# Performance work log

Measured on AMD Instinct MI355X. Metric: run time of the kernel, lower is better.

## Reference

```python
import jax, jax.numpy as jnp
import numpy as np

TEMPERATURE = 8.0  # sqrt(d_k=64)
NEG_INF = -1000000000.0

B, H, S, D = 2, 16, 2048, 64


def setup_inputs() -> dict:
    key = jax.random.key(0)
    kq, kk, kv, knm, km = jax.random.split(key, 5)
    q = jax.random.normal(kq, (B, H, S, D), dtype=jnp.float32)
    k = jax.random.normal(kk, (B, H, S, D), dtype=jnp.float32)
    v = jax.random.normal(kv, (B, H, S, D), dtype=jnp.float32)
    new_mask = jax.random.uniform(knm, (B, 1, S, S), dtype=jnp.float32)
    mask = jax.random.randint(km, (B, 1, S, S), 0, 2).astype(jnp.bool_)
    return {"q": q, "k": k, "v": v, "new_mask": new_mask, "mask": mask}


def reference(q, k, v, new_mask, mask):
    # scores: [B,H,S,S] = (q/temp) @ k^T
    attn = jnp.einsum("bhqd,bhkd->bhqk", q / TEMPERATURE, k)
    attn = jnp.where(mask, NEG_INF, attn)
    attn = jax.nn.softmax(attn, axis=-1)
    attn = attn * new_mask  # post-softmax elementwise mask-mul
    output = jnp.einsum("bhqk,bhkd->bhqd", attn, v)
    return (output, attn)
```

## Files before the change

kernel.cpp:

```cpp
#include <hip/hip_runtime.h>
#include <hip/hip_bf16.h>


#define Bsz 2
#define Hn 16
#define Sn 2048
#define Dn 64
#define NEG_INF -1000000000.0f
#define MBOUND 20.0f

typedef __attribute__((ext_vector_type(8))) short bf16x8;
typedef __attribute__((ext_vector_type(4))) float f32x4;

__device__ __forceinline__ unsigned short f2bf(float x) {
  unsigned u = __builtin_bit_cast(unsigned, x);
  u += 0x7fffu + ((u >> 16) & 1u);
  return (unsigned short)(u >> 16);
}
__device__ __forceinline__ float bf2f(unsigned short x) {
  return __builtin_bit_cast(float, ((unsigned)x) << 16);
}
__device__ __forceinline__ bf16x8 lds8(const unsigned short* p) {
  union { ushort4 h[2]; bf16x8 v; } u;
  u.h[0] = *(const ushort4*)p;
  u.h[1] = *(const ushort4*)(p + 4);
  return u.v;
}
__device__ __forceinline__ int swz(int r, int c) {
  return r * 68 + (c ^ ((r & 7) << 3));
}

__global__ __launch_bounds__(256, 4) void attn_single(
    const float* __restrict__ qg, const float* __restrict__ kg,
    const float* __restrict__ vg, const float* __restrict__ nmg,
    const int* __restrict__ mg, float* __restrict__ outO,
    unsigned short* __restrict__ wa, float* __restrict__ wil)
{
  __shared__ __align__(16) unsigned short qs[64 * 68];
  __shared__ __align__(16) unsigned short ks[64 * 68];
  __shared__ __align__(16) unsigned short vts[64 * 68];
  __shared__ __align__(16) unsigned short ps[4 * 16 * 68];

  const int tid = threadIdx.x;
  const int wv = tid >> 6;
  const int lane = tid & 63;
  const int lg = lane >> 4, li = lane & 15;
  const int qb = blockIdx.x * 64;
  const int h = blockIdx.y, b = blockIdx.z;
  const int bh = b * Hn + h;

  const float* qp  = qg + (size_t)bh * Sn * Dn;
  const float* kp  = kg + (size_t)bh * Sn * Dn;
  const float* vp  = vg + (size_t)bh * Sn * Dn;
  const float* nmb = nmg + (size_t)b * Sn * Sn;
  const int*   mb  = mg  + (size_t)b * Sn * Sn;
  float* outOp = outO + (size_t)bh * Sn * Dn;

  #pragma unroll
  for (int i = 0; i < 4; ++i) {
    int slot = tid + i * 256;
    int r = slot >> 4, c = (slot & 15) << 2;
    float4 f = *(const float4*)(qp + (size_t)(qb + r) * Dn + c);
    ushort4 u = { f2bf(f.x*0.125f), f2bf(f.y*0.125f), f2bf(f.z*0.125f), f2bf(f.w*0.125f) };
    *(ushort4*)&qs[swz(r, c)] = u;
  }
  __syncthreads();
  bf16x8 aq0 = lds8(&qs[swz(wv*16 + li, lg*8)]);
  bf16x8 aq1 = lds8(&qs[swz(wv*16 + li, 32 + lg*8)]);

  float lp[4] = {0.f, 0.f, 0.f, 0.f};
  f32x4 oa[4];
  #pragma unroll
  for (int n = 0; n < 4; ++n) { f32x4 z = {0.f,0.f,0.f,0.f}; oa[n] = z; }

  float4 fk[4], fv[4];
  #pragma unroll
  for (int i = 0; i < 4; ++i) {
    int slot = tid + i * 256;
    int r = slot >> 4, c = (slot & 15) << 2;
    fk[i] = *(const float4*)(kp + (size_t)r * Dn + c);
    fv[i] = *(const float4*)(vp + (size_t)r * Dn + c);
  }

  for (int k0 = 0; k0 < Sn; k0 += 64) {
    #pragma unroll
    for (int i = 0; i < 4; ++i) {
      int slot = tid + i * 256;
      int r = slot >> 4, c = (slot & 15) << 2;
      ushort4 u = { f2bf(fk[i].x), f2bf(fk[i].y), f2bf(fk[i].z), f2bf(fk[i].w) };
      *(ushort4*)&ks[swz(r, c)] = u;
      vts[swz(c+0, r)] = f2bf(fv[i].x);
      vts[swz(c+1, r)] = f2bf(fv[i].y);
      vts[swz(c+2, r)] = f2bf(fv[i].z);
      vts[swz(c+3, r)] = f2bf(fv[i].w);
    }
    __syncthreads();
    if (k0 + 64 < Sn) {
      #pragma unroll
      for (int i = 0; i < 4; ++i) {
        int slot = tid + i * 256;
        int r = slot >> 4, c = (slot & 15) << 2;
        fk[i] = *(const float4*)(kp + (size_t)(k0 + 64 + r) * Dn + c);
        fv[i] = *(const float4*)(vp + (size_t)(k0 + 64 + r) * Dn + c);
      }
    }

    f32x4 acc[4];
    #pragma unroll
    for (int n = 0; n < 4; ++n) { f32x4 z = {0.f,0.f,0.f,0.f}; acc[n] = z; }
    #pragma unroll
    for (int n = 0; n < 4; ++n) {
      acc[n] = __builtin_amdgcn_mfma_f32_16x16x32_bf16(aq0, lds8(&ks[swz(n*16+li, lg*8)]),    acc[n], 0, 0, 0);
      acc[n] = __builtin_amdgcn_mfma_f32_16x16x32_bf16(aq1, lds8(&ks[swz(n*16+li, 32+lg*8)]), acc[n], 0, 0, 0);
    }

    #pragma unroll
    for (int r = 0; r < 4; ++r) {
      int row = lg*4 + r;
      int grow = qb + wv*16 + row;
      size_t rowo = (size_t)grow * Sn + k0 + li;
      const int* mp = mb + rowo;
      const float* nmp = nmb + rowo;
      float psum = 0.f;
      #pragma unroll
      for (int n = 0; n < 4; ++n) {
        float p = mp[n*16] ? 0.f : __expf(acc[n][r] - MBOUND);
        psum += p;
        float a = p * nmp[n*16];
        ps[wv*1088 + swz(row, n*16 + li)] = f2bf(a);
      }
      lp[r] += psum;
    }
    asm volatile("s_waitcnt lgkmcnt(0)" ::: "memory");

    #pragma unroll
    for (int kk = 0; kk < 2; ++kk) {
      bf16x8 ap8 = lds8(&ps[wv*1088 + swz(li, kk*32 + lg*8)]);
      #pragma unroll
      for (int n2 = 0; n2 < 4; ++n2) {
        oa[n2] = __builtin_amdgcn_mfma_f32_16x16x32_bf16(
            ap8, lds8(&vts[swz(n2*16 + li, kk*32 + lg*8)]), oa[n2], 0, 0, 0);
      }
    }

    #pragma unroll
    for (int it = 0; it < 2; ++it) {
      int row = it*8 + (lane >> 3);
      int cseg = (lane & 7) * 8;
      bf16x8 w = lds8(&ps[wv*1088 + swz(row, cseg)]);
      *(bf16x8*)(wa + ((size_t)bh * Sn + qb + wv*16 + row) * Sn + k0 + cseg) = w;
    }
    __syncthreads();
  }

  float il[4];
  #pragma unroll
  for (int r = 0; r < 4; ++r) {
    float l = lp[r];
    #pragma unroll
    for (int d2 = 1; d2 < 16; d2 <<= 1) l += __shfl_xor(l, d2);
    il[r] = (l > 0.f) ? 1.f / l : 0.f;
  }
  #pragma unroll
  for (int n2 = 0; n2 < 4; ++n2)
    #pragma unroll
    for (int r = 0; r < 4; ++r)
      outOp[(size_t)(qb + wv*16 + lg*4 + r) * Dn + n2*16 + li] = oa[n2][r] * il[r];
  if (li == 0) {
    #pragma unroll
    for (int r = 0; r < 4; ++r)
      wil[(size_t)bh * Sn + qb + wv*16 + lg*4 + r] = il[r];
  }
}

__global__ __launch_bounds__(256) void attn_rescale(
    const unsigned short* __restrict__ wa, const float* __restrict__ wil,
    float* __restrict__ outA)
{
  size_t g = (size_t)blockIdx.x * 256 + threadIdx.x;
  #pragma unroll 2
  for (int it = 0; it < 8; ++it, g += 2097152) {
    size_t e = g * 8;
    float s = wil[e >> 11];
    bf16x8 v = *(const bf16x8*)(wa + e);
    float4 o0 = { bf2f((unsigned short)v[0]) * s, bf2f((unsigned short)v[1]) * s,
                  bf2f((unsigned short)v[2]) * s, bf2f((unsigned short)v[3]) * s };
    float4 o1 = { bf2f((unsigned short)v[4]) * s, bf2f((unsigned short)v[5]) * s,
                  bf2f((unsigned short)v[6]) * s, bf2f((unsigned short)v[7]) * s };
    *(float4*)(outA + e) = o0;
    *(float4*)(outA + e + 4) = o1;
  }
}

__global__ __launch_bounds__(256, 4) void attn_fused(
    const float* __restrict__ qg, const float* __restrict__ kg,
    const float* __restrict__ vg, const float* __restrict__ nmg,
    const int* __restrict__ mg, float* __restrict__ outg)
{
  __shared__ unsigned short qs[64][72];
  __shared__ unsigned short ks[64][72];
  __shared__ unsigned short vts[64][72];
  __shared__ unsigned short ps[4][16][72];

  const int tid = threadIdx.x;
  const int wv = tid >> 6;
  const int lane = tid & 63;
  const int lg = lane >> 4, li = lane & 15;
  const int qb = blockIdx.x * 64;
  const int h = blockIdx.y, b = blockIdx.z;

  const float* qp  = qg + (size_t)(b*Hn + h) * Sn * Dn;
  const float* kp  = kg + (size_t)(b*Hn + h) * Sn * Dn;
  const float* vp  = vg + (size_t)(b*Hn + h) * Sn * Dn;
  const float* nmb = nmg + (size_t)b * Sn * Sn;
  const int*   mb  = mg  + (size_t)b * Sn * Sn;
  float* outO = outg + (size_t)(b*Hn + h) * Sn * Dn;
  float* outA = outg + (size_t)Bsz*Hn*Sn*Dn + (size_t)(b*Hn + h) * Sn * Sn;

  #pragma unroll
  for (int i = 0; i < 4; ++i) {
    int slot = tid + i*256;
    int r = slot >> 4, c = (slot & 15) << 2;
    float4 f = *(const float4*)(qp + (size_t)(qb + r)*Dn + c);
    ushort4 u = { f2bf(f.x*0.125f), f2bf(f.y*0.125f), f2bf(f.z*0.125f), f2bf(f.w*0.125f) };
    *(ushort4*)&qs[r][c] = u;
  }
  __syncthreads();
  bf16x8 aq0 = lds8(&qs[wv*16 + li][lg*8]);
  bf16x8 aq1 = lds8(&qs[wv*16 + li][32 + lg*8]);

  float mr[4] = {-INFINITY, -INFINITY, -INFINITY, -INFINITY};
  float lr[4] = {0.f, 0.f, 0.f, 0.f};

  for (int k0 = 0; k0 < Sn; k0 += 64) {
    __syncthreads();
    #pragma unroll
    for (int i = 0; i < 4; ++i) {
      int slot = tid + i*256;
      int r = slot >> 4, c = (slot & 15) << 2;
      float4 f = *(const float4*)(kp + (size_t)(k0 + r)*Dn + c);
      ushort4 u = { f2bf(f.x), f2bf(f.y), f2bf(f.z), f2bf(f.w) };
      *(ushort4*)&ks[r][c] = u;
    }
    __syncthreads();
    f32x4 acc[4];
    #pragma unroll
    for (int n = 0; n < 4; ++n) { f32x4 z = {0.f,0.f,0.f,0.f}; acc[n] = z; }
    #pragma unroll
    for (int n = 0; n < 4; ++n) {
      acc[n] = __builtin_amdgcn_mfma_f32_16x16x32_bf16(aq0, lds8(&ks[n*16+li][lg*8]),    acc[n], 0, 0, 0);
      acc[n] = __builtin_amdgcn_mfma_f32_16x16x32_bf16(aq1, lds8(&ks[n*16+li][32+lg*8]), acc[n], 0, 0, 0);
    }
    #pragma unroll
    for (int r = 0; r < 4; ++r) {
      int grow = qb + wv*16 + lg*4 + r;
      const int* mp = mb + (size_t)grow*Sn + k0 + li;
      float s0 = mp[0]  ? NEG_INF : acc[0][r];
      float s1 = mp[16] ? NEG_INF : acc[1][r];
      float s2 = mp[32] ? NEG_INF : acc[2][r];
      float s3 = mp[48] ? NEG_INF : acc[3][r];
      float tmax = fmaxf(fmaxf(s0, s1), fmaxf(s2, s3));
      #pragma unroll
      for (int d2 = 1; d2 < 16; d2 <<= 1) tmax = fmaxf(tmax, __shfl_xor(tmax, d2));
      float mn = fmaxf(mr[r], tmax);
      float se = __expf(s0 - mn) + __expf(s1 - mn) + __expf(s2 - mn) + __expf(s3 - mn);
      #pragma unroll
      for (int d2 = 1; d2 < 16; d2 <<= 1) se += __shfl_xor(se, d2);
      lr[r] = lr[r] * __expf(mr[r] - mn) + se;
      mr[r] = mn;
    }
  }
  float il[4];
  #pragma unroll
  for (int r = 0; r < 4; ++r) il[r] = 1.0f / lr[r];
  f32x4 oa[4];
  #pragma unroll
  for (int n = 0; n < 4; ++n) { f32x4 z = {0.f,0.f,0.f,0.f}; oa[n] = z; }

  for (int k0 = 0; k0 < Sn; k0 += 64) {
    __syncthreads();
    #pragma unroll
    for (int i = 0; i < 4; ++i) {
      int slot = tid + i*256;
      int r = slot >> 4, c = (slot & 15) << 2;
      float4 f = *(const float4*)(kp + (size_t)(k0 + r)*Dn + c);
      ushort4 u = { f2bf(f.x), f2bf(f.y), f2bf(f.z), f2bf(f.w) };
      *(ushort4*)&ks[r][c] = u;
      float4 g = *(const float4*)(vp + (size_t)(k0 + r)*Dn + c);
      vts[c+0][r] = f2bf(g.x);
      vts[c+1][r] = f2bf(g.y);
      vts[c+2][r] = f2bf(g.z);
      vts[c+3][r] = f2bf(g.w);
    }
    __syncthreads();
    f32x4 acc[4];
    #pragma unroll
    for (int n = 0; n < 4; ++n) { f32x4 z = {0.f,0.f,0.f,0.f}; acc[n] = z; }
    #pragma unroll
    for (int n = 0; n < 4; ++n) {
      acc[n] = __builtin_amdgcn_mfma_f32_16x16x32_bf16(aq0, lds8(&ks[n*16+li][lg*8]),    acc[n], 0, 0, 0);
      acc[n] = __builtin_amdgcn_mfma_f32_16x16x32_bf16(aq1, lds8(&ks[n*16+li][32+lg*8]), acc[n], 0, 0, 0);
    }
    #pragma unroll
    for (int r = 0; r < 4; ++r) {
      int grow = qb + wv*16 + lg*4 + r;
      const size_t rowo = (size_t)grow*Sn + k0 + li;
      const int* mp = mb + rowo;
      const float* nmp = nmb + rowo;
      float* ap = outA + rowo;
      #pragma unroll
      for (int n = 0; n < 4; ++n) {
        float p = mp[n*16] ? 0.f : __expf(acc[n][r] - mr[r]) * il[r];
        float a = p * nmp[n*16];
        ap[n*16] = a;
        ps[wv][lg*4 + r][n*16 + li] = f2bf(a);
      }
    }
    asm volatile("s_waitcnt lgkmcnt(0)" ::: "memory");
    #pragma unroll
    for (int kk = 0; kk < 2; ++kk) {
      bf16x8 ap8 = lds8(&ps[wv][li][kk*32 + lg*8]);
      #pragma unroll
      for (int n2 = 0; n2 < 4; ++n2) {
        oa[n2] = __builtin_amdgcn_mfma_f32_16x16x32_bf16(
            ap8, lds8(&vts[n2*16 + li][kk*32 + lg*8]), oa[n2], 0, 0, 0);
      }
    }
  }
  #pragma unroll
  for (int n2 = 0; n2 < 4; ++n2)
    #pragma unroll
    for (int r = 0; r < 4; ++r)
      outO[(size_t)(qb + wv*16 + lg*4 + r)*Dn + n2*16 + li] = oa[n2][r];
}

extern "C" void kernel_launch(void* const* d_in, const int* in_sizes, int n_in,
                              void* d_out, int out_size, void* d_ws, size_t ws_size,
                              hipStream_t stream) {
  const float* q  = (const float*)d_in[0];
  const float* k  = (const float*)d_in[1];
  const float* v  = (const float*)d_in[2];
  const float* nm = (const float*)d_in[3];
  const int*   m  = (const int*)d_in[4];
  float* out = (float*)d_out;
  const size_t o_elems = (size_t)Bsz*Hn*Sn*Dn;
  const size_t a_elems = (size_t)Bsz*Hn*Sn*Sn;
  const size_t need = 262144 + a_elems * 2;
  dim3 grid(Sn / 64, Hn, Bsz);
  if (ws_size >= need) {
    float* wil = (float*)d_ws;
    unsigned short* wa = (unsigned short*)((char*)d_ws + 262144);
    attn_single<<<grid, dim3(256), 0, stream>>>(q, k, v, nm, m, out, wa, wil);
    attn_rescale<<<dim3(8192), dim3(256), 0, stream>>>(wa, wil, out + o_elems);
  } else {
    attn_fused<<<grid, dim3(256), 0, stream>>>(q, k, v, nm, m, out);
  }
}
```

Measured before the change: 1.200 ms.

## Prefetch mask tiles into registers, remap block IDs, and prioritize MFMA waves

Loads the next k-tile's boolean mask and new_mask values into registers one iteration ahead, so those global loads overlap the QK and PV MFMAs instead of stalling the softmax step. Flattens the grid to 1D and applies an XCD-aware block-ID swizzle so consecutive blocks on one die share the same head and reuse K/V in L2. Wraps the MFMA sections in s_setprio to favour compute waves. The cost is 32 extra VGPRs per thread, which may lower occupancy under the launch bounds.

```diff
diff --git a/kernel.cpp b/kernel.cpp
--- a/kernel.cpp
+++ b/kernel.cpp
@@ -45,9 +45,13 @@
   const int wv = tid >> 6;
   const int lane = tid & 63;
   const int lg = lane >> 4, li = lane & 15;
-  const int qb = blockIdx.x * 64;
-  const int h = blockIdx.y, b = blockIdx.z;
-  const int bh = b * Hn + h;
+
+  const int id = blockIdx.x;
+  const int swzid = (id & 7) * 128 + (id >> 3);
+  const int qx = swzid & 31;
+  const int bh = swzid >> 5;
+  const int b = bh >> 4;
+  const int qb = qx * 64;
 
   const float* qp  = qg + (size_t)bh * Sn * Dn;
   const float* kp  = kg + (size_t)bh * Sn * Dn;
@@ -80,6 +84,17 @@
     int r = slot >> 4, c = (slot & 15) << 2;
     fk[i] = *(const float4*)(kp + (size_t)r * Dn + c);
     fv[i] = *(const float4*)(vp + (size_t)r * Dn + c);
+  }
+  int   pmv[16];
+  float pnmv[16];
+  #pragma unroll
+  for (int r = 0; r < 4; ++r) {
+    size_t rowo = (size_t)(qb + wv*16 + lg*4 + r) * Sn + li;
+    #pragma unroll
+    for (int n = 0; n < 4; ++n) {
+      pmv[r*4 + n]  = mb[rowo + n*16];
+      pnmv[r*4 + n] = nmb[rowo + n*16];
+    }
   }
 
   for (int k0 = 0; k0 < Sn; k0 += 64) {
@@ -108,31 +123,41 @@
     f32x4 acc[4];
     #pragma unroll
     for (int n = 0; n < 4; ++n) { f32x4 z = {0.f,0.f,0.f,0.f}; acc[n] = z; }
+    __builtin_amdgcn_s_setprio(1);
     #pragma unroll
     for (int n = 0; n < 4; ++n) {
       acc[n] = __builtin_amdgcn_mfma_f32_16x16x32_bf16(aq0, lds8(&ks[swz(n*16+li, lg*8)]),    acc[n], 0, 0, 0);
       acc[n] = __builtin_amdgcn_mfma_f32_16x16x32_bf16(aq1, lds8(&ks[swz(n*16+li, 32+lg*8)]), acc[n], 0, 0, 0);
     }
+    __builtin_amdgcn_s_setprio(0);
 
     #pragma unroll
     for (int r = 0; r < 4; ++r) {
       int row = lg*4 + r;
-      int grow = qb + wv*16 + row;
-      size_t rowo = (size_t)grow * Sn + k0 + li;
-      const int* mp = mb + rowo;
-      const float* nmp = nmb + rowo;
       float psum = 0.f;
       #pragma unroll
       for (int n = 0; n < 4; ++n) {
-        float p = mp[n*16] ? 0.f : __expf(acc[n][r] - MBOUND);
+        float p = pmv[r*4 + n] ? 0.f : __expf(acc[n][r] - MBOUND);
         psum += p;
-        float a = p * nmp[n*16];
+        float a = p * pnmv[r*4 + n];
         ps[wv*1088 + swz(row, n*16 + li)] = f2bf(a);
       }
       lp[r] += psum;
     }
+    if (k0 + 64 < Sn) {
+      #pragma unroll
+      for (int r = 0; r < 4; ++r) {
+        size_t rowo = (size_t)(qb + wv*16 + lg*4 + r) * Sn + (k0 + 64) + li;
+        #pragma unroll
+        for (int n = 0; n < 4; ++n) {
+          pmv[r*4 + n]  = mb[rowo + n*16];
+          pnmv[r*4 + n] = nmb[rowo + n*16];
+        }
+      }
+    }
     asm volatile("s_waitcnt lgkmcnt(0)" ::: "memory");
 
+    __builtin_amdgcn_s_setprio(1);
     #pragma unroll
     for (int kk = 0; kk < 2; ++kk) {
       bf16x8 ap8 = lds8(&ps[wv*1088 + swz(li, kk*32 + lg*8)]);
@@ -142,6 +167,7 @@
             ap8, lds8(&vts[swz(n2*16 + li, kk*32 + lg*8)]), oa[n2], 0, 0, 0);
       }
     }
+    __builtin_amdgcn_s_setprio(0);
 
     #pragma unroll
     for (int it = 0; it < 2; ++it) {
@@ -346,13 +372,13 @@
   const size_t o_elems = (size_t)Bsz*Hn*Sn*Dn;
   const size_t a_elems = (size_t)Bsz*Hn*Sn*Sn;
   const size_t need = 262144 + a_elems * 2;
-  dim3 grid(Sn / 64, Hn, Bsz);
   if (ws_size >= need) {
     float* wil = (float*)d_ws;
     unsigned short* wa = (unsigned short*)((char*)d_ws + 262144);
-    attn_single<<<grid, dim3(256), 0, stream>>>(q, k, v, nm, m, out, wa, wil);
+    attn_single<<<dim3(1024), dim3(256), 0, stream>>>(q, k, v, nm, m, out, wa, wil);
     attn_rescale<<<dim3(8192), dim3(256), 0, stream>>>(wa, wil, out + o_elems);
   } else {
+    dim3 grid(Sn / 64, Hn, Bsz);
     attn_fused<<<grid, dim3(256), 0, stream>>>(q, k, v, nm, m, out);
   }
 }
```

Measured after the change: 1.618 ms. +34.8%, slower.
